# Performance work log

Measured on AMD Instinct MI355X. Metric: run time of the kernel, lower is better.

## Reference

```python
import jax, jax.numpy as jnp
import numpy as np

EMBED = 1024  # point_net_embedding_dim
H1, H2 = 512, 256  # head_hidden_layer_sizes


def _init(key, shape, fan_in):
    return jax.random.normal(key, shape, dtype=jnp.float32) / jnp.sqrt(jnp.float32(fan_in))


def setup_inputs() -> dict:
    key = jax.random.key(0)
    ks = jax.random.split(key, 13)
    B, N = 256, 1024
    x = jax.random.normal(ks[0], (B, N, 3), dtype=jnp.float32)
    # PointNet shared per-point MLP: 3 -> 64 -> 128 -> EMBED (ReLU), max-pool over points
    W1 = _init(ks[1], (3, 64), 3);        b1 = jnp.zeros((64,), jnp.float32)
    W2 = _init(ks[2], (64, 128), 64);     b2 = jnp.zeros((128,), jnp.float32)
    W3 = _init(ks[3], (128, EMBED), 128); b3 = jnp.zeros((EMBED,), jnp.float32)
    # Head MLP: EMBED -> 512 -> 256 -> 9 (no final activation)
    Wh1 = _init(ks[4], (EMBED, H1), EMBED); bh1 = jnp.zeros((H1,), jnp.float32)
    Wh2 = _init(ks[5], (H1, H2), H1);       bh2 = jnp.zeros((H2,), jnp.float32)
    Wh3 = _init(ks[6], (H2, 9), H2);        bh3 = jnp.zeros((9,), jnp.float32)
    return {"x": x, "W1": W1, "b1": b1, "W2": W2, "b2": b2, "W3": W3, "b3": b3,
            "Wh1": Wh1, "bh1": bh1, "Wh2": Wh2, "bh2": bh2, "Wh3": Wh3, "bh3": bh3}


def svd_projection(M):
    # Project raw 3x3 matrices onto SO(3): R = U diag(1,1,det(U V^T)) V^T
    U, S, Vh = jnp.linalg.svd(M, full_matrices=False)
    det = jnp.linalg.det(jnp.einsum('...ij,...jk->...ik', U, Vh))
    d = jnp.stack([jnp.ones_like(det), jnp.ones_like(det), det], axis=-1)  # [..., 3]
    return jnp.einsum('...ij,...j,...jk->...ik', U, d, Vh)


def reference(x, W1, b1, W2, b2, W3, b3, Wh1, bh1, Wh2, bh2, Wh3, bh3):
    # Shared per-point MLP (ReLU), final_activation=ReLU, then max-pool over points
    h = jax.nn.relu(x @ W1 + b1)          # [B, N, 64]
    h = jax.nn.relu(h @ W2 + b2)          # [B, N, 128]
    h = jax.nn.relu(h @ W3 + b3)          # [B, N, EMBED]
    g = jnp.max(h, axis=-2)               # [B, EMBED] global feature
    # Head MLP -> raw 3x3
    z = jax.nn.relu(g @ Wh1 + bh1)
    z = jax.nn.relu(z @ Wh2 + bh2)
    raw = (z @ Wh3 + bh3).reshape(*x.shape[:-2], 3, 3)
    return svd_projection(raw)
```

## Files before the change

kernel.cpp:

```cpp
#include <hip/hip_runtime.h>
#include <math.h>

typedef _Float16 f16;
typedef _Float16 f16x8 __attribute__((ext_vector_type(8)));
typedef float f32x4 __attribute__((ext_vector_type(4)));

#define H2_STRIDE 136

__global__ __launch_bounds__(256) void prep_weights(
    const float* __restrict__ W1, const float* __restrict__ b1,
    const float* __restrict__ W2, const float* __restrict__ W3,
    f16* __restrict__ W2t, f16* __restrict__ W3t, float* __restrict__ wpk)
{
    int idx = blockIdx.x * 256 + threadIdx.x;
    int stride = gridDim.x * 256;
    for (int i = idx; i < 1024 * 128; i += stride) {
        int c = i >> 7, k = i & 127;
        W3t[i] = (f16)W3[k * 1024 + c];
    }
    for (int i = idx; i < 128 * 64; i += stride) {
        int c = i >> 6, k = i & 63;
        W2t[i] = (f16)W2[k * 128 + c];
    }
    if (idx < 256) {
        int k = idx >> 2, c = idx & 3;
        wpk[idx] = (c < 3) ? W1[c * 64 + k] : b1[k];
    }
}

__global__ __launch_bounds__(512, 2) void pointnet_fused(
    const float* __restrict__ x,
    const float* __restrict__ wpk,
    const f16* __restrict__ W2t,
    const float* __restrict__ b2,
    const f16* __restrict__ W3t,
    const float* __restrict__ b3,
    float* __restrict__ g)
{
    __shared__ float xs[1024 * 3];
    __shared__ __align__(16) float wls[288];
    __shared__ float b2s[128];
    __shared__ __align__(16) f16 h2s[2][128 * H2_STRIDE];

    int b = blockIdx.x;
    int tid = threadIdx.x;
    int lane = tid & 63, w = tid >> 6;
    int lrow = lane & 15, quad = lane >> 4;
    int wr2 = w & 3, wc2 = w >> 2;

    f16x8 bf3[8][4];
    {
        const f16* base = W3t + (size_t)(w * 128 + lrow) * 128 + quad * 8;
#pragma unroll
        for (int ct = 0; ct < 8; ct++)
#pragma unroll
            for (int kc = 0; kc < 4; kc++)
                bf3[ct][kc] = *(const f16x8*)(base + ct * 16 * 128 + kc * 32);
    }
    f16x8 bf2[4][2];
    {
        const f16* base = W2t + (size_t)(wc2 * 64 + lrow) * 64 + quad * 8;
#pragma unroll
        for (int ct = 0; ct < 4; ct++)
#pragma unroll
            for (int kc2 = 0; kc2 < 2; kc2++)
                bf2[ct][kc2] = *(const f16x8*)(base + ct * 16 * 64 + kc2 * 32);
    }

    {
        const float* xb = x + (size_t)b * 3072;
        for (int i = tid; i < 3072; i += 512) xs[i] = xb[i];
        if (tid < 256) {
            int k = tid >> 2, c = tid & 3;
            wls[(k + (k >> 3)) * 4 + c] = wpk[tid];
        }
        if (tid >= 256 && tid < 384) b2s[tid - 256] = b2[tid - 256];
    }
    __syncthreads();

    const f32x4 z4 = {0.f, 0.f, 0.f, 0.f};
    float cmax[8];
#pragma unroll
    for (int ct = 0; ct < 8; ct++) cmax[ct] = -3.0e38f;

    auto phaseA = [&](int chunk) {
        f16* hb = h2s[chunk & 1];
        int p0 = chunk * 128 + wr2 * 32 + lrow;
        float x00 = xs[p0 * 3], x01 = xs[p0 * 3 + 1], x02 = xs[p0 * 3 + 2];
        int p1 = p0 + 16;
        float x10 = xs[p1 * 3], x11 = xs[p1 * 3 + 1], x12 = xs[p1 * 3 + 2];
        f32x4 acc2[2][4];
#pragma unroll
        for (int kc2 = 0; kc2 < 2; kc2++) {
            f16x8 af2[2];
#pragma unroll
            for (int j = 0; j < 8; j++) {
                int k = kc2 * 32 + quad * 8 + j;
                f32x4 wv = *(const f32x4*)&wls[(k + (k >> 3)) * 4];
                float v0 = fmaf(x02, wv[2], fmaf(x01, wv[1], fmaf(x00, wv[0], wv[3])));
                float v1 = fmaf(x12, wv[2], fmaf(x11, wv[1], fmaf(x10, wv[0], wv[3])));
                af2[0][j] = (f16)fmaxf(v0, 0.f);
                af2[1][j] = (f16)fmaxf(v1, 0.f);
            }
#pragma unroll
            for (int rt = 0; rt < 2; rt++)
#pragma unroll
                for (int ct = 0; ct < 4; ct++)
                    acc2[rt][ct] = __builtin_amdgcn_mfma_f32_16x16x32_f16(
                        af2[rt], bf2[ct][kc2], kc2 ? acc2[rt][ct] : z4, 0, 0, 0);
        }
#pragma unroll
        for (int rt = 0; rt < 2; rt++)
#pragma unroll
            for (int ct = 0; ct < 4; ct++) {
                int col = wc2 * 64 + ct * 16 + lrow;
                float bb = b2s[col];
                int rowb = wr2 * 32 + rt * 16 + quad * 4;
#pragma unroll
                for (int r = 0; r < 4; r++)
                    hb[(rowb + r) * H2_STRIDE + col] = (f16)fmaxf(acc2[rt][ct][r] + bb, 0.f);
            }
    };

    auto phaseB = [&](int chunk) {
        const f16* hb = h2s[chunk & 1];
#pragma unroll
        for (int rt = 0; rt < 8; rt++) {
            f32x4 acc[8];
#pragma unroll
            for (int kc = 0; kc < 4; kc++) {
                f16x8 af = *(const f16x8*)(hb + (rt * 16 + lrow) * H2_STRIDE + kc * 32 + quad * 8);
#pragma unroll
                for (int ct = 0; ct < 8; ct++)
                    acc[ct] = __builtin_amdgcn_mfma_f32_16x16x32_f16(
                        af, bf3[ct][kc], kc ? acc[ct] : z4, 0, 0, 0);
            }
#pragma unroll
            for (int ct = 0; ct < 8; ct++) {
                float m01 = fmaxf(acc[ct][0], acc[ct][1]);
                float m23 = fmaxf(acc[ct][2], acc[ct][3]);
                cmax[ct] = fmaxf(cmax[ct], fmaxf(m01, m23));
            }
        }
    };

    phaseA(0);
    __syncthreads();
#pragma unroll 1
    for (int c = 0; c < 7; c++) {
        phaseA(c + 1);
        phaseB(c);
        __syncthreads();
    }
    phaseB(7);

#pragma unroll
    for (int ct = 0; ct < 8; ct++) {
        cmax[ct] = fmaxf(cmax[ct], __shfl_xor(cmax[ct], 16, 64));
        cmax[ct] = fmaxf(cmax[ct], __shfl_xor(cmax[ct], 32, 64));
    }
    if (quad == 0) {
#pragma unroll
        for (int ct = 0; ct < 8; ct++) {
            int cg = w * 128 + ct * 16 + lrow;
            g[(size_t)b * 1024 + cg] = fmaxf(cmax[ct] + b3[cg], 0.f);
        }
    }
}

__device__ inline void jrot(double S[3][3], double V[3][3], int p, int q)
{
    double apq = S[p][q];
    if (fabs(apq) < 1e-36) return;
    double tau = (S[q][q] - S[p][p]) / (2.0 * apq);
    double t = (tau >= 0.0 ? 1.0 : -1.0) / (fabs(tau) + sqrt(1.0 + tau * tau));
    double c = 1.0 / sqrt(1.0 + t * t);
    double s = t * c;
    for (int k = 0; k < 3; k++) {
        double skp = S[k][p], skq = S[k][q];
        S[k][p] = c * skp - s * skq;  S[k][q] = s * skp + c * skq;
    }
    for (int k = 0; k < 3; k++) {
        double spk = S[p][k], sqk = S[q][k];
        S[p][k] = c * spk - s * sqk;  S[q][k] = s * spk + c * sqk;
    }
    for (int k = 0; k < 3; k++) {
        double vkp = V[k][p], vkq = V[k][q];
        V[k][p] = c * vkp - s * vkq;  V[k][q] = s * vkp + c * vkq;
    }
}

__device__ void svd_so3(const float* Mf, float* Rout)
{
    double M[3][3], S[3][3], V[3][3];
    for (int i = 0; i < 3; i++)
        for (int j = 0; j < 3; j++) M[i][j] = (double)Mf[3 * i + j];
    for (int i = 0; i < 3; i++)
        for (int j = 0; j < 3; j++)
            S[i][j] = M[0][i] * M[0][j] + M[1][i] * M[1][j] + M[2][i] * M[2][j];
    for (int i = 0; i < 3; i++)
        for (int j = 0; j < 3; j++) V[i][j] = (i == j) ? 1.0 : 0.0;
    for (int it = 0; it < 10; it++) {
        jrot(S, V, 0, 1); jrot(S, V, 0, 2); jrot(S, V, 1, 2);
    }
    double lam[3] = {S[0][0], S[1][1], S[2][2]};
    int i0 = 0, i1 = 1, i2 = 2, tt;
    if (lam[i0] < lam[i1]) { tt = i0; i0 = i1; i1 = tt; }
    if (lam[i0] < lam[i2]) { tt = i0; i0 = i2; i2 = tt; }
    if (lam[i1] < lam[i2]) { tt = i1; i1 = i2; i2 = tt; }
    double v0[3], v1[3], v2[3];
    for (int k = 0; k < 3; k++) { v0[k] = V[k][i0]; v1[k] = V[k][i1]; v2[k] = V[k][i2]; }
    double u1[3], u2[3], u3[3];
    for (int i = 0; i < 3; i++) u1[i] = M[i][0] * v0[0] + M[i][1] * v0[1] + M[i][2] * v0[2];
    double n1 = sqrt(u1[0] * u1[0] + u1[1] * u1[1] + u1[2] * u1[2]) + 1e-300;
    for (int i = 0; i < 3; i++) u1[i] /= n1;
    for (int i = 0; i < 3; i++) u2[i] = M[i][0] * v1[0] + M[i][1] * v1[1] + M[i][2] * v1[2];
    double d12 = u1[0] * u2[0] + u1[1] * u2[1] + u1[2] * u2[2];
    for (int i = 0; i < 3; i++) u2[i] -= d12 * u1[i];
    double n2 = sqrt(u2[0] * u2[0] + u2[1] * u2[1] + u2[2] * u2[2]) + 1e-300;
    for (int i = 0; i < 3; i++) u2[i] /= n2;
    u3[0] = u1[1] * u2[2] - u1[2] * u2[1];
    u3[1] = u1[2] * u2[0] - u1[0] * u2[2];
    u3[2] = u1[0] * u2[1] - u1[1] * u2[0];
    double c12x = v1[1] * v2[2] - v1[2] * v2[1];
    double c12y = v1[2] * v2[0] - v1[0] * v2[2];
    double c12z = v1[0] * v2[1] - v1[1] * v2[0];
    double detV = v0[0] * c12x + v0[1] * c12y + v0[2] * c12z;
    for (int i = 0; i < 3; i++)
        for (int j = 0; j < 3; j++)
            Rout[3 * i + j] = (float)(u1[i] * v0[j] + u2[i] * v1[j] + detV * u3[i] * v2[j]);
}

__global__ __launch_bounds__(512) void head_batched(
    const float* __restrict__ g,
    const float* __restrict__ Wh1, const float* __restrict__ bh1,
    const float* __restrict__ Wh2, const float* __restrict__ bh2,
    const float* __restrict__ Wh3, const float* __restrict__ bh3,
    float* __restrict__ out)
{
    __shared__ float gsm[2][1024];
    __shared__ float z1p[4][2][512];
    __shared__ float z1s[2][512];
    __shared__ float z2p[8][2][256];
    __shared__ float z2s[2][256];
    __shared__ float l3p[16][2][9];
    __shared__ float wh3s[2304];
    __shared__ float raw[2][12];

    int b0 = blockIdx.x * 2;
    int tid = threadIdx.x;
    int roff = (blockIdx.x * 131) & 255;

    for (int i = tid; i < 2048; i += 512)
        gsm[i >> 10][i & 1023] = g[(size_t)(b0 + (i >> 10)) * 1024 + (i & 1023)];
    for (int i = tid; i < 2304; i += 512) wh3s[i] = Wh3[i];
    __syncthreads();

    {
        int cg = tid & 127;
        int ks = tid >> 7;
        int k0 = ks * 256;
        f32x4 a0 = {0.f, 0.f, 0.f, 0.f}, a1 = {0.f, 0.f, 0.f, 0.f};
        const float* wp = Wh1 + cg * 4;
#pragma unroll 4
        for (int kk = 0; kk < 256; kk++) {
            int k = k0 + ((kk + roff) & 255);
            f32x4 wv = *(const f32x4*)(wp + (size_t)k * 512);
            float g0 = gsm[0][k], g1 = gsm[1][k];
            a0[0] = fmaf(g0, wv[0], a0[0]);  a1[0] = fmaf(g1, wv[0], a1[0]);
            a0[1] = fmaf(g0, wv[1], a0[1]);  a1[1] = fmaf(g1, wv[1], a1[1]);
            a0[2] = fmaf(g0, wv[2], a0[2]);  a1[2] = fmaf(g1, wv[2], a1[2]);
            a0[3] = fmaf(g0, wv[3], a0[3]);  a1[3] = fmaf(g1, wv[3], a1[3]);
        }
        *(f32x4*)&z1p[ks][0][cg * 4] = a0;
        *(f32x4*)&z1p[ks][1][cg * 4] = a1;
    }
    __syncthreads();
    for (int i = tid; i < 1024; i += 512) {
        int r = i >> 9, col = i & 511;
        float v = bh1[col] + z1p[0][r][col] + z1p[1][r][col]
                           + z1p[2][r][col] + z1p[3][r][col];
        z1s[r][col] = fmaxf(v, 0.f);
    }
    __syncthreads();

    {
        int cg = tid & 63;
        int ks = tid >> 6;
        int k0 = ks * 64;
        int roff2 = roff & 63;
        f32x4 a0 = {0.f, 0.f, 0.f, 0.f}, a1 = {0.f, 0.f, 0.f, 0.f};
        const float* wp = Wh2 + cg * 4;
#pragma unroll 4
        for (int kk = 0; kk < 64; kk++) {
            int k = k0 + ((kk + roff2) & 63);
            f32x4 wv = *(const f32x4*)(wp + (size_t)k * 256);
            float z0 = z1s[0][k], z1v = z1s[1][k];
            a0[0] = fmaf(z0, wv[0], a0[0]);  a1[0] = fmaf(z1v, wv[0], a1[0]);
            a0[1] = fmaf(z0, wv[1], a0[1]);  a1[1] = fmaf(z1v, wv[1], a1[1]);
            a0[2] = fmaf(z0, wv[2], a0[2]);  a1[2] = fmaf(z1v, wv[2], a1[2]);
            a0[3] = fmaf(z0, wv[3], a0[3]);  a1[3] = fmaf(z1v, wv[3], a1[3]);
        }
        *(f32x4*)&z2p[ks][0][cg * 4] = a0;
        *(f32x4*)&z2p[ks][1][cg * 4] = a1;
    }
    __syncthreads();
    {
        int r = tid >> 8, col = tid & 255;
        float v = bh2[col];
#pragma unroll
        for (int j = 0; j < 8; j++) v += z2p[j][r][col];
        z2s[r][col] = fmaxf(v, 0.f);
    }
    __syncthreads();

    if (tid < 288) {
        int r = tid / 144, rem = tid - r * 144;
        int c = rem % 9, ks = rem / 9;
        float a = 0.f;
#pragma unroll
        for (int k = 0; k < 16; k++)
            a = fmaf(z2s[r][ks * 16 + k], wh3s[(ks * 16 + k) * 9 + c], a);
        l3p[ks][r][c] = a;
    }
    __syncthreads();
    if (tid < 18) {
        int r = tid / 9, c = tid - r * 9;
        float a = bh3[c];
#pragma unroll
        for (int j = 0; j < 16; j++) a += l3p[j][r][c];
        raw[r][c] = a;
    }
    __syncthreads();

    if (tid < 2)
        svd_so3(&raw[tid][0], out + (size_t)(b0 + tid) * 9);
}

extern "C" void kernel_launch(void* const* d_in, const int* in_sizes, int n_in,
                              void* d_out, int out_size, void* d_ws, size_t ws_size,
                              hipStream_t stream)
{
    const float* x   = (const float*)d_in[0];
    const float* W1  = (const float*)d_in[1];
    const float* b1  = (const float*)d_in[2];
    const float* W2  = (const float*)d_in[3];
    const float* b2  = (const float*)d_in[4];
    const float* W3  = (const float*)d_in[5];
    const float* b3  = (const float*)d_in[6];
    const float* Wh1 = (const float*)d_in[7];
    const float* bh1 = (const float*)d_in[8];
    const float* Wh2 = (const float*)d_in[9];
    const float* bh2 = (const float*)d_in[10];
    const float* Wh3 = (const float*)d_in[11];
    const float* bh3 = (const float*)d_in[12];
    float* out = (float*)d_out;

    char* ws = (char*)d_ws;
    f16*   W2t = (f16*)ws;
    f16*   W3t = (f16*)(ws + 65536);
    float* wpk = (float*)(ws + 524288);
    float* g   = (float*)(ws + 1048576);

    prep_weights<<<128, 256, 0, stream>>>(W1, b1, W2, W3, W2t, W3t, wpk);
    pointnet_fused<<<256, 512, 0, stream>>>(x, wpk, W2t, b2, W3t, b3, g);
    head_batched<<<128, 512, 0, stream>>>(g, Wh1, bh1, Wh2, bh2, Wh3, bh3, out);
}
```

Measured before the change: 172.5 us.

## Fold weight transpose/convert into fused PointNet kernel and reorder phase loop

Removes the separate prep_weights launch. Each block now reads the fp32 W1/W2/W3 directly, converts them to fp16 and transposes them through the shared h2s buffer, then loads its MFMA B-fragments from there. The main loop also swaps the order so phaseB runs before phaseA for the next chunk. This drops one kernel launch and a global round-trip, but every one of the 256 blocks now repeats the W3 transpose with strided global reads, and the setup adds several extra barriers.

```diff
diff --git a/kernel.cpp b/kernel.cpp
--- a/kernel.cpp
+++ b/kernel.cpp
@@ -2,38 +2,19 @@
 #include <math.h>
 
 typedef _Float16 f16;
+typedef _Float16 f16x2 __attribute__((ext_vector_type(2)));
 typedef _Float16 f16x8 __attribute__((ext_vector_type(8)));
 typedef float f32x4 __attribute__((ext_vector_type(4)));
 
 #define H2_STRIDE 136
 
-__global__ __launch_bounds__(256) void prep_weights(
-    const float* __restrict__ W1, const float* __restrict__ b1,
-    const float* __restrict__ W2, const float* __restrict__ W3,
-    f16* __restrict__ W2t, f16* __restrict__ W3t, float* __restrict__ wpk)
-{
-    int idx = blockIdx.x * 256 + threadIdx.x;
-    int stride = gridDim.x * 256;
-    for (int i = idx; i < 1024 * 128; i += stride) {
-        int c = i >> 7, k = i & 127;
-        W3t[i] = (f16)W3[k * 1024 + c];
-    }
-    for (int i = idx; i < 128 * 64; i += stride) {
-        int c = i >> 6, k = i & 63;
-        W2t[i] = (f16)W2[k * 128 + c];
-    }
-    if (idx < 256) {
-        int k = idx >> 2, c = idx & 3;
-        wpk[idx] = (c < 3) ? W1[c * 64 + k] : b1[k];
-    }
-}
-
 __global__ __launch_bounds__(512, 2) void pointnet_fused(
     const float* __restrict__ x,
-    const float* __restrict__ wpk,
-    const f16* __restrict__ W2t,
+    const float* __restrict__ W1,
+    const float* __restrict__ b1,
+    const float* __restrict__ W2,
     const float* __restrict__ b2,
-    const f16* __restrict__ W3t,
+    const float* __restrict__ W3,
     const float* __restrict__ b3,
     float* __restrict__ g)
 {
@@ -48,35 +29,67 @@
     int lrow = lane & 15, quad = lane >> 4;
     int wr2 = w & 3, wc2 = w >> 2;
 
-    f16x8 bf3[8][4];
-    {
-        const f16* base = W3t + (size_t)(w * 128 + lrow) * 128 + quad * 8;
-#pragma unroll
-        for (int ct = 0; ct < 8; ct++)
-#pragma unroll
-            for (int kc = 0; kc < 4; kc++)
-                bf3[ct][kc] = *(const f16x8*)(base + ct * 16 * 128 + kc * 32);
-    }
-    f16x8 bf2[4][2];
-    {
-        const f16* base = W2t + (size_t)(wc2 * 64 + lrow) * 64 + quad * 8;
-#pragma unroll
-        for (int ct = 0; ct < 4; ct++)
-#pragma unroll
-            for (int kc2 = 0; kc2 < 2; kc2++)
-                bf2[ct][kc2] = *(const f16x8*)(base + ct * 16 * 64 + kc2 * 32);
-    }
+    f16* flat = &h2s[0][0];
 
     {
         const float* xb = x + (size_t)b * 3072;
         for (int i = tid; i < 3072; i += 512) xs[i] = xb[i];
         if (tid < 256) {
             int k = tid >> 2, c = tid & 3;
-            wls[(k + (k >> 3)) * 4 + c] = wpk[tid];
+            wls[(k + (k >> 3)) * 4 + c] = (c < 3) ? W1[c * 64 + k] : b1[k];
         }
         if (tid >= 256 && tid < 384) b2s[tid - 256] = b2[tid - 256];
     }
-    __syncthreads();
+
+    f16x8 bf3[8][4];
+    {
+        int cl2 = tid & 255;
+        int kh  = tid >> 8;
+        for (int r = 0; r < 4; r++) {
+            const float* src = W3 + r * 256 + cl2;
+            f16* dst = flat + (size_t)cl2 * H2_STRIDE;
+#pragma unroll 8
+            for (int p = 0; p < 32; p++) {
+                int k = kh * 64 + (((p + cl2) & 31) * 2);
+                f16x2 pk = { (f16)src[(size_t)k * 1024],
+                             (f16)src[(size_t)(k + 1) * 1024] };
+                *(f16x2*)(dst + k) = pk;
+            }
+            __syncthreads();
+            if ((w >> 1) == r) {
+                const f16* base = flat + (size_t)((w & 1) * 128 + lrow) * H2_STRIDE + quad * 8;
+#pragma unroll
+                for (int ct = 0; ct < 8; ct++)
+#pragma unroll
+                    for (int kc = 0; kc < 4; kc++)
+                        bf3[ct][kc] = *(const f16x8*)(base + ct * 16 * H2_STRIDE + kc * 32);
+            }
+            __syncthreads();
+        }
+    }
+
+    f16x8 bf2[4][2];
+    {
+        int cl = tid & 127;
+        int kh = tid >> 7;
+        const float* src = W2 + cl;
+        f16* dst = flat + (size_t)cl * H2_STRIDE;
+#pragma unroll 8
+        for (int p = 0; p < 8; p++) {
+            int k = kh * 16 + (((p + cl) & 7) * 2);
+            f16x2 pk = { (f16)src[(size_t)k * 128],
+                         (f16)src[(size_t)(k + 1) * 128] };
+            *(f16x2*)(dst + k) = pk;
+        }
+        __syncthreads();
+        const f16* base = flat + (size_t)(wc2 * 64 + lrow) * H2_STRIDE + quad * 8;
+#pragma unroll
+        for (int ct = 0; ct < 4; ct++)
+#pragma unroll
+            for (int kc2 = 0; kc2 < 2; kc2++)
+                bf2[ct][kc2] = *(const f16x8*)(base + ct * 16 * H2_STRIDE + kc2 * 32);
+        __syncthreads();
+    }
 
     const f32x4 z4 = {0.f, 0.f, 0.f, 0.f};
     float cmax[8];
@@ -148,8 +161,8 @@
     __syncthreads();
 #pragma unroll 1
     for (int c = 0; c < 7; c++) {
+        phaseB(c);
         phaseA(c + 1);
-        phaseB(c);
         __syncthreads();
     }
     phaseB(7);
@@ -356,13 +369,8 @@
     const float* bh3 = (const float*)d_in[12];
     float* out = (float*)d_out;
 
-    char* ws = (char*)d_ws;
-    f16*   W2t = (f16*)ws;
-    f16*   W3t = (f16*)(ws + 65536);
-    float* wpk = (float*)(ws + 524288);
-    float* g   = (float*)(ws + 1048576);
-
-    prep_weights<<<128, 256, 0, stream>>>(W1, b1, W2, W3, W2t, W3t, wpk);
-    pointnet_fused<<<256, 512, 0, stream>>>(x, wpk, W2t, b2, W3t, b3, g);
+    float* g = (float*)d_ws;
+
+    pointnet_fused<<<256, 512, 0, stream>>>(x, W1, b1, W2, b2, W3, b3, g);
     head_batched<<<128, 512, 0, stream>>>(g, Wh1, bh1, Wh2, bh2, Wh3, bh3, out);
 }
```

Measured after the change: 269.5 us. 1.56x slower.

## Merge prep, pointnet and head into one cooperative kernel with grid syncs

Applied to the files above, without the earlier changes.

Replaces the three separate kernel launches with a single cooperative kernel that runs weight prep, the fused PointNet, and the head MLP as phases separated by grid-wide barriers. Shared memory is reused through a union-sized buffer. The aim is to remove inter-kernel launch gaps and drain/refill bubbles. In exchange it adds grid.sync cost and limits occupancy, since all 256 blocks must be co-resident. It keeps the three-kernel path as a fallback if the cooperative launch fails.

```diff
diff --git a/kernel.cpp b/kernel.cpp
--- a/kernel.cpp
+++ b/kernel.cpp
@@ -1,5 +1,8 @@
 #include <hip/hip_runtime.h>
+#include <hip/hip_cooperative_groups.h>
 #include <math.h>
+
+namespace cg = cooperative_groups;
 
 typedef _Float16 f16;
 typedef _Float16 f16x8 __attribute__((ext_vector_type(8)));
@@ -7,13 +10,28 @@
 
 #define H2_STRIDE 136
 
-__global__ __launch_bounds__(256) void prep_weights(
+struct PnLds {
+    __align__(16) f16 h2s[2][128 * H2_STRIDE];
+    float xs[3072];
+    __align__(16) float wls[288];
+    float b2s[128];
+};
+struct HdLds {
+    float gsm[2][1024];
+    float z1p[4][2][512];
+    float z1s[2][512];
+    float z2p[8][2][256];
+    float z2s[2][256];
+    float l3p[16][2][9];
+    float wh3s[2304];
+    float raw[2][12];
+};
+
+__device__ void phase_prep(int idx, int stride,
     const float* __restrict__ W1, const float* __restrict__ b1,
     const float* __restrict__ W2, const float* __restrict__ W3,
     f16* __restrict__ W2t, f16* __restrict__ W3t, float* __restrict__ wpk)
 {
-    int idx = blockIdx.x * 256 + threadIdx.x;
-    int stride = gridDim.x * 256;
     for (int i = idx; i < 1024 * 128; i += stride) {
         int c = i >> 7, k = i & 127;
         W3t[i] = (f16)W3[k * 1024 + c];
@@ -28,22 +46,12 @@
     }
 }
 
-__global__ __launch_bounds__(512, 2) void pointnet_fused(
-    const float* __restrict__ x,
-    const float* __restrict__ wpk,
-    const f16* __restrict__ W2t,
-    const float* __restrict__ b2,
-    const f16* __restrict__ W3t,
-    const float* __restrict__ b3,
+__device__ void phase_pointnet(PnLds& L, int b, int tid,
+    const float* __restrict__ x, const float* __restrict__ wpk,
+    const f16* __restrict__ W2t, const float* __restrict__ b2,
+    const f16* __restrict__ W3t, const float* __restrict__ b3,
     float* __restrict__ g)
 {
-    __shared__ float xs[1024 * 3];
-    __shared__ __align__(16) float wls[288];
-    __shared__ float b2s[128];
-    __shared__ __align__(16) f16 h2s[2][128 * H2_STRIDE];
-
-    int b = blockIdx.x;
-    int tid = threadIdx.x;
     int lane = tid & 63, w = tid >> 6;
     int lrow = lane & 15, quad = lane >> 4;
     int wr2 = w & 3, wc2 = w >> 2;
@@ -69,12 +77,12 @@
 
     {
         const float* xb = x + (size_t)b * 3072;
-        for (int i = tid; i < 3072; i += 512) xs[i] = xb[i];
+        for (int i = tid; i < 3072; i += 512) L.xs[i] = xb[i];
         if (tid < 256) {
             int k = tid >> 2, c = tid & 3;
-            wls[(k + (k >> 3)) * 4 + c] = wpk[tid];
-        }
-        if (tid >= 256 && tid < 384) b2s[tid - 256] = b2[tid - 256];
+            L.wls[(k + (k >> 3)) * 4 + c] = wpk[tid];
+        }
+        if (tid >= 256 && tid < 384) L.b2s[tid - 256] = b2[tid - 256];
     }
     __syncthreads();
 
@@ -84,11 +92,11 @@
     for (int ct = 0; ct < 8; ct++) cmax[ct] = -3.0e38f;
 
     auto phaseA = [&](int chunk) {
-        f16* hb = h2s[chunk & 1];
+        f16* hb = L.h2s[chunk & 1];
         int p0 = chunk * 128 + wr2 * 32 + lrow;
-        float x00 = xs[p0 * 3], x01 = xs[p0 * 3 + 1], x02 = xs[p0 * 3 + 2];
+        float x00 = L.xs[p0 * 3], x01 = L.xs[p0 * 3 + 1], x02 = L.xs[p0 * 3 + 2];
         int p1 = p0 + 16;
-        float x10 = xs[p1 * 3], x11 = xs[p1 * 3 + 1], x12 = xs[p1 * 3 + 2];
+        float x10 = L.xs[p1 * 3], x11 = L.xs[p1 * 3 + 1], x12 = L.xs[p1 * 3 + 2];
         f32x4 acc2[2][4];
 #pragma unroll
         for (int kc2 = 0; kc2 < 2; kc2++) {
@@ -96,7 +104,7 @@
 #pragma unroll
             for (int j = 0; j < 8; j++) {
                 int k = kc2 * 32 + quad * 8 + j;
-                f32x4 wv = *(const f32x4*)&wls[(k + (k >> 3)) * 4];
+                f32x4 wv = *(const f32x4*)&L.wls[(k + (k >> 3)) * 4];
                 float v0 = fmaf(x02, wv[2], fmaf(x01, wv[1], fmaf(x00, wv[0], wv[3])));
                 float v1 = fmaf(x12, wv[2], fmaf(x11, wv[1], fmaf(x10, wv[0], wv[3])));
                 af2[0][j] = (f16)fmaxf(v0, 0.f);
@@ -114,7 +122,7 @@
 #pragma unroll
             for (int ct = 0; ct < 4; ct++) {
                 int col = wc2 * 64 + ct * 16 + lrow;
-                float bb = b2s[col];
+                float bb = L.b2s[col];
                 int rowb = wr2 * 32 + rt * 16 + quad * 4;
 #pragma unroll
                 for (int r = 0; r < 4; r++)
@@ -123,7 +131,7 @@
     };
 
     auto phaseB = [&](int chunk) {
-        const f16* hb = h2s[chunk & 1];
+        const f16* hb = L.h2s[chunk & 1];
 #pragma unroll
         for (int rt = 0; rt < 8; rt++) {
             f32x4 acc[8];
@@ -231,29 +239,19 @@
             Rout[3 * i + j] = (float)(u1[i] * v0[j] + u2[i] * v1[j] + detV * u3[i] * v2[j]);
 }
 
-__global__ __launch_bounds__(512) void head_batched(
+__device__ void phase_head(HdLds& L, int bb, int tid,
     const float* __restrict__ g,
     const float* __restrict__ Wh1, const float* __restrict__ bh1,
     const float* __restrict__ Wh2, const float* __restrict__ bh2,
     const float* __restrict__ Wh3, const float* __restrict__ bh3,
     float* __restrict__ out)
 {
-    __shared__ float gsm[2][1024];
-    __shared__ float z1p[4][2][512];
-    __shared__ float z1s[2][512];
-    __shared__ float z2p[8][2][256];
-    __shared__ float z2s[2][256];
-    __shared__ float l3p[16][2][9];
-    __shared__ float wh3s[2304];
-    __shared__ float raw[2][12];
-
-    int b0 = blockIdx.x * 2;
-    int tid = threadIdx.x;
-    int roff = (blockIdx.x * 131) & 255;
+    int b0 = bb * 2;
+    int roff = (bb * 131) & 255;
 
     for (int i = tid; i < 2048; i += 512)
-        gsm[i >> 10][i & 1023] = g[(size_t)(b0 + (i >> 10)) * 1024 + (i & 1023)];
-    for (int i = tid; i < 2304; i += 512) wh3s[i] = Wh3[i];
+        L.gsm[i >> 10][i & 1023] = g[(size_t)(b0 + (i >> 10)) * 1024 + (i & 1023)];
+    for (int i = tid; i < 2304; i += 512) L.wh3s[i] = Wh3[i];
     __syncthreads();
 
     {
@@ -266,21 +264,21 @@
         for (int kk = 0; kk < 256; kk++) {
             int k = k0 + ((kk + roff) & 255);
             f32x4 wv = *(const f32x4*)(wp + (size_t)k * 512);
-            float g0 = gsm[0][k], g1 = gsm[1][k];
+            float g0 = L.gsm[0][k], g1 = L.gsm[1][k];
             a0[0] = fmaf(g0, wv[0], a0[0]);  a1[0] = fmaf(g1, wv[0], a1[0]);
             a0[1] = fmaf(g0, wv[1], a0[1]);  a1[1] = fmaf(g1, wv[1], a1[1]);
             a0[2] = fmaf(g0, wv[2], a0[2]);  a1[2] = fmaf(g1, wv[2], a1[2]);
             a0[3] = fmaf(g0, wv[3], a0[3]);  a1[3] = fmaf(g1, wv[3], a1[3]);
         }
-        *(f32x4*)&z1p[ks][0][cg * 4] = a0;
-        *(f32x4*)&z1p[ks][1][cg * 4] = a1;
+        *(f32x4*)&L.z1p[ks][0][cg * 4] = a0;
+        *(f32x4*)&L.z1p[ks][1][cg * 4] = a1;
     }
     __syncthreads();
     for (int i = tid; i < 1024; i += 512) {
         int r = i >> 9, col = i & 511;
-        float v = bh1[col] + z1p[0][r][col] + z1p[1][r][col]
-                           + z1p[2][r][col] + z1p[3][r][col];
-        z1s[r][col] = fmaxf(v, 0.f);
+        float v = bh1[col] + L.z1p[0][r][col] + L.z1p[1][r][col]
+                           + L.z1p[2][r][col] + L.z1p[3][r][col];
+        L.z1s[r][col] = fmaxf(v, 0.f);
     }
     __syncthreads();
 
@@ -295,22 +293,22 @@
         for (int kk = 0; kk < 64; kk++) {
             int k = k0 + ((kk + roff2) & 63);
             f32x4 wv = *(const f32x4*)(wp + (size_t)k * 256);
-            float z0 = z1s[0][k], z1v = z1s[1][k];
+            float z0 = L.z1s[0][k], z1v = L.z1s[1][k];
             a0[0] = fmaf(z0, wv[0], a0[0]);  a1[0] = fmaf(z1v, wv[0], a1[0]);
             a0[1] = fmaf(z0, wv[1], a0[1]);  a1[1] = fmaf(z1v, wv[1], a1[1]);
             a0[2] = fmaf(z0, wv[2], a0[2]);  a1[2] = fmaf(z1v, wv[2], a1[2]);
             a0[3] = fmaf(z0, wv[3], a0[3]);  a1[3] = fmaf(z1v, wv[3], a1[3]);
         }
-        *(f32x4*)&z2p[ks][0][cg * 4] = a0;
-        *(f32x4*)&z2p[ks][1][cg * 4] = a1;
+        *(f32x4*)&L.z2p[ks][0][cg * 4] = a0;
+        *(f32x4*)&L.z2p[ks][1][cg * 4] = a1;
     }
     __syncthreads();
     {
         int r = tid >> 8, col = tid & 255;
         float v = bh2[col];
 #pragma unroll
-        for (int j = 0; j < 8; j++) v += z2p[j][r][col];
-        z2s[r][col] = fmaxf(v, 0.f);
+        for (int j = 0; j < 8; j++) v += L.z2p[j][r][col];
+        L.z2s[r][col] = fmaxf(v, 0.f);
     }
     __syncthreads();
 
@@ -320,21 +318,83 @@
         float a = 0.f;
 #pragma unroll
         for (int k = 0; k < 16; k++)
-            a = fmaf(z2s[r][ks * 16 + k], wh3s[(ks * 16 + k) * 9 + c], a);
-        l3p[ks][r][c] = a;
+            a = fmaf(L.z2s[r][ks * 16 + k], L.wh3s[(ks * 16 + k) * 9 + c], a);
+        L.l3p[ks][r][c] = a;
     }
     __syncthreads();
     if (tid < 18) {
         int r = tid / 9, c = tid - r * 9;
         float a = bh3[c];
 #pragma unroll
-        for (int j = 0; j < 16; j++) a += l3p[j][r][c];
-        raw[r][c] = a;
+        for (int j = 0; j < 16; j++) a += L.l3p[j][r][c];
+        L.raw[r][c] = a;
     }
     __syncthreads();
 
     if (tid < 2)
-        svd_so3(&raw[tid][0], out + (size_t)(b0 + tid) * 9);
+        svd_so3(&L.raw[tid][0], out + (size_t)(b0 + tid) * 9);
+}
+
+__global__ __launch_bounds__(512, 2) void meganet(
+    const float* __restrict__ x,
+    const float* __restrict__ W1, const float* __restrict__ b1,
+    const float* __restrict__ W2, const float* __restrict__ b2,
+    const float* __restrict__ W3, const float* __restrict__ b3,
+    const float* __restrict__ Wh1, const float* __restrict__ bh1,
+    const float* __restrict__ Wh2, const float* __restrict__ bh2,
+    const float* __restrict__ Wh3, const float* __restrict__ bh3,
+    f16* __restrict__ W2t, f16* __restrict__ W3t, float* __restrict__ wpk,
+    float* __restrict__ g, float* __restrict__ out)
+{
+    __shared__ __align__(16) char smem[sizeof(PnLds) > sizeof(HdLds) ? sizeof(PnLds) : sizeof(HdLds)];
+    cg::grid_group grid = cg::this_grid();
+
+    int tid = threadIdx.x;
+    int bid = blockIdx.x;
+
+    phase_prep(bid * 512 + tid, 256 * 512, W1, b1, W2, W3, W2t, W3t, wpk);
+
+    __threadfence();
+    grid.sync();
+
+    phase_pointnet(*reinterpret_cast<PnLds*>(smem), bid, tid, x, wpk, W2t, b2, W3t, b3, g);
+
+    __threadfence();
+    grid.sync();
+
+    if (bid < 128)
+        phase_head(*reinterpret_cast<HdLds*>(smem), bid, tid, g,
+                   Wh1, bh1, Wh2, bh2, Wh3, bh3, out);
+}
+
+__global__ __launch_bounds__(256) void prep_k(
+    const float* __restrict__ W1, const float* __restrict__ b1,
+    const float* __restrict__ W2, const float* __restrict__ W3,
+    f16* __restrict__ W2t, f16* __restrict__ W3t, float* __restrict__ wpk)
+{
+    phase_prep(blockIdx.x * 256 + threadIdx.x, gridDim.x * 256,
+               W1, b1, W2, W3, W2t, W3t, wpk);
+}
+
+__global__ __launch_bounds__(512, 2) void pointnet_k(
+    const float* __restrict__ x, const float* __restrict__ wpk,
+    const f16* __restrict__ W2t, const float* __restrict__ b2,
+    const f16* __restrict__ W3t, const float* __restrict__ b3,
+    float* __restrict__ g)
+{
+    __shared__ PnLds L;
+    phase_pointnet(L, blockIdx.x, threadIdx.x, x, wpk, W2t, b2, W3t, b3, g);
+}
+
+__global__ __launch_bounds__(512) void head_k(
+    const float* __restrict__ g,
+    const float* __restrict__ Wh1, const float* __restrict__ bh1,
+    const float* __restrict__ Wh2, const float* __restrict__ bh2,
+    const float* __restrict__ Wh3, const float* __restrict__ bh3,
+    float* __restrict__ out)
+{
+    __shared__ HdLds L;
+    phase_head(L, blockIdx.x, threadIdx.x, g, Wh1, bh1, Wh2, bh2, Wh3, bh3, out);
 }
 
 extern "C" void kernel_launch(void* const* d_in, const int* in_sizes, int n_in,
@@ -362,7 +422,18 @@
     float* wpk = (float*)(ws + 524288);
     float* g   = (float*)(ws + 1048576);
 
-    prep_weights<<<128, 256, 0, stream>>>(W1, b1, W2, W3, W2t, W3t, wpk);
-    pointnet_fused<<<256, 512, 0, stream>>>(x, wpk, W2t, b2, W3t, b3, g);
-    head_batched<<<128, 512, 0, stream>>>(g, Wh1, bh1, Wh2, bh2, Wh3, bh3, out);
-}
+    void* args[] = {
+        (void*)&x, (void*)&W1, (void*)&b1, (void*)&W2, (void*)&b2,
+        (void*)&W3, (void*)&b3, (void*)&Wh1, (void*)&bh1, (void*)&Wh2,
+        (void*)&bh2, (void*)&Wh3, (void*)&bh3,
+        (void*)&W2t, (void*)&W3t, (void*)&wpk, (void*)&g, (void*)&out
+    };
+    hipError_t err = hipLaunchCooperativeKernel(
+        (const void*)meganet, dim3(256), dim3(512), args, 0, stream);
+
+    if (err != hipSuccess) {
+        prep_k<<<128, 256, 0, stream>>>(W1, b1, W2, W3, W2t, W3t, wpk);
+        pointnet_k<<<256, 512, 0, stream>>>(x, wpk, W2t, b2, W3t, b3, g);
+        head_k<<<128, 512, 0, stream>>>(g, Wh1, bh1, Wh2, bh2, Wh3, bh3, out);
+    }
+}
```

New measurement: 349.5 us. +102.5%, slower.
